# Kernel tuning notes

Measured on AMD Instinct MI355X. Metric: run time of the kernel, lower is better.

The kernel has to match this reference:

```python
import jax, jax.numpy as jnp
import numpy as np

NUM_CLASSES = 26
PERCENTILE = 95.0
BIG = jnp.float32(1e10)


def _erode(m):
    # scipy-style binary erosion with cross structuring element, border_value=0
    p = jnp.pad(m, 1, constant_values=False)
    return m & p[:-2, 1:-1] & p[2:, 1:-1] & p[1:-1, :-2] & p[1:-1, 2:]


def _boundary(m):
    return m & ~_erode(m)


def _edt(edge):
    # Exact Euclidean distance transform to nearest True pixel of `edge` [H, W].
    # Two-pass separable formulation (rows then columns), fully vectorized.
    H, W = edge.shape
    r = jnp.arange(H)
    rd2 = ((r[:, None] - r[None, :]) ** 2).astype(jnp.float32)  # [H, H']
    # g[i, j] = min over i' with edge[i', j] of (i - i')^2
    g = jnp.min(jnp.where(edge[None, :, :], rd2[:, :, None], BIG), axis=1)  # [H, W]
    c = jnp.arange(W)
    cd2 = ((c[:, None] - c[None, :]) ** 2).astype(jnp.float32)  # [W', W]
    # dt2[i, j] = min over j' of g[i, j'] + (j' - j)^2
    dt2 = jnp.min(g[:, :, None] + cd2[None, :, :], axis=1)  # [H, W]
    return jnp.sqrt(dt2)


def _pct95(dists, mask):
    # np.percentile(dists[mask], 95) with linear interpolation; nan if mask empty
    n = jnp.sum(mask)
    s = jnp.sort(jnp.where(mask, dists, jnp.inf))
    idx = (PERCENTILE / 100.0) * (n.astype(jnp.float32) - 1.0)
    idx = jnp.maximum(idx, 0.0)
    lo = jnp.floor(idx).astype(jnp.int32)
    hi = jnp.ceil(idx).astype(jnp.int32)
    vlo = s[lo]
    vhi = s[hi]
    val = vlo + (vhi - vlo) * (idx - jnp.floor(idx))
    return jnp.where(n > 0, val, jnp.nan)


def _hd_pair(pl, tl, c):
    # 95th-percentile symmetric Hausdorff between pred/target binary masks of class c
    pm = pl == c
    tm = tl == c
    pe = _boundary(pm)
    te = _boundary(tm)
    dt_t = _edt(te)  # distance to target boundary
    dt_p = _edt(pe)  # distance to pred boundary
    d_pt = _pct95(dt_t.ravel(), pe.ravel())  # pred-edge -> target-edge
    d_tp = _pct95(dt_p.ravel(), te.ravel())  # target-edge -> pred-edge
    return jnp.maximum(d_pt, d_tp)


def setup_inputs() -> dict:
    key = jax.random.key(0)
    k1, k2 = jax.random.split(key)
    predicted = jax.random.normal(k1, (2, NUM_CLASSES, 256, 256), dtype=jnp.float32)
    target = jax.random.normal(k2, (2, NUM_CLASSES, 256, 256), dtype=jnp.float32)
    return {"predicted": predicted, "target": target}


def reference(predicted, target):
    probs = jax.nn.softmax(predicted, axis=1)
    pl = jnp.argmax(probs, axis=1)   # [B, H, W]
    tl = jnp.argmax(target, axis=1)  # [B, H, W]

    def per_class(c):
        hd = jax.vmap(lambda p, t: _hd_pair(p, t, c))(pl, tl)  # [B]
        present = jnp.any(tl == c, axis=(1, 2))                # [B]
        return hd, present

    hds, pres = jax.lax.map(per_class, jnp.arange(NUM_CLASSES))  # [C, B]
    presf = pres.astype(jnp.float32)
    num = jnp.sum(jnp.where(pres, hds, 0.0), axis=0)  # [B]
    den = jnp.sum(presf, axis=0)                      # [B]
    batch_means = num / jnp.maximum(den, 1.0)
    valid = den > 0
    total = jnp.sum(jnp.where(valid, batch_means, 0.0)) / jnp.maximum(
        jnp.sum(valid.astype(jnp.float32)), 1.0)
    return jnp.where(jnp.any(valid), total, jnp.inf)
```

## Files before the change

kernel.cpp:

```cpp
#include <hip/hip_runtime.h>
#include <math.h>

#define HW 65536
#define NC 26
#define NB 2

#define PL_OFF    0
#define TL_OFF    131072
#define CNT_OFF   262144
#define RES_OFF   263424
#define BMP_OFF   264192
#define LISTP_OFF 1116160
#define LISTT_OFF 7931904
#define MINP_OFF  14747648
#define MINT_OFF  28379136

__global__ void k_labels(const float4* __restrict__ pred, const float4* __restrict__ targ,
                         uchar4* __restrict__ pl, uchar4* __restrict__ tl,
                         unsigned int* __restrict__ cnt) {
    int tid = threadIdx.x;
    if (blockIdx.x == 0) {
        for (int i = tid; i < 320; i += 128) cnt[i] = 0;
    }
    int idx = blockIdx.x * 128 + tid;
    if (idx >= (NB * HW / 4)) return;
    int b = idx >> 14, q = idx & 16383;
    const float4* p = pred + ((size_t)b * NC << 14) + q;
    const float4* t = targ + ((size_t)b * NC << 14) + q;
    float4 bp = p[0]; uchar4 ap = {0, 0, 0, 0};
    float4 bt = t[0]; uchar4 at = {0, 0, 0, 0};
#pragma unroll
    for (int c = 1; c < NC; ++c) {
        float4 vp = p[(size_t)c << 14];
        if (vp.x > bp.x) { bp.x = vp.x; ap.x = (unsigned char)c; }
        if (vp.y > bp.y) { bp.y = vp.y; ap.y = (unsigned char)c; }
        if (vp.z > bp.z) { bp.z = vp.z; ap.z = (unsigned char)c; }
        if (vp.w > bp.w) { bp.w = vp.w; ap.w = (unsigned char)c; }
        float4 vt = t[(size_t)c << 14];
        if (vt.x > bt.x) { bt.x = vt.x; at.x = (unsigned char)c; }
        if (vt.y > bt.y) { bt.y = vt.y; at.y = (unsigned char)c; }
        if (vt.z > bt.z) { bt.z = vt.z; at.z = (unsigned char)c; }
        if (vt.w > bt.w) { bt.w = vt.w; at.w = (unsigned char)c; }
    }
    pl[idx] = ap;
    tl[idx] = at;
}

__device__ __forceinline__ bool is_boundary(const unsigned char* __restrict__ L, int hw, int c) {
    int y = hw >> 8, x = hw & 255;
    if (y == 0 || y == 255 || x == 0 || x == 255) return true;
    return (int)L[hw - 256] != c || (int)L[hw + 256] != c ||
           (int)L[hw - 1]   != c || (int)L[hw + 1]   != c;
}

__global__ void k_rowbm(const unsigned char* __restrict__ pl,
                        const unsigned char* __restrict__ tl,
                        unsigned int* __restrict__ bmp,
                        unsigned int* __restrict__ cnt,
                        unsigned short* __restrict__ listP,
                        unsigned short* __restrict__ listT) {
    __shared__ unsigned bm[52][8];
    __shared__ unsigned lh[52];
    __shared__ unsigned lb[52];
    int tid = threadIdx.x;
    int b = blockIdx.x >> 8, y = blockIdx.x & 255;
    for (int i = tid; i < 416; i += 256) ((unsigned*)bm)[i] = 0;
    if (tid < 52) lh[tid] = 0;
    __syncthreads();
    const unsigned char* Lp = pl + (b << 16);
    const unsigned char* Lt = tl + (b << 16);
    int hw = (y << 8) | tid;
    int cp = Lp[hw];
    int ct = Lt[hw];
    bool bnp = is_boundary(Lp, hw, cp);
    bool bnt = is_boundary(Lt, hw, ct);
    unsigned rp = 0, rt = 0;
    if (bnp) {
        atomicOr(&bm[cp][tid >> 5], 1u << (tid & 31));
        rp = atomicAdd(&lh[cp], 1u);
    }
    if (bnt) {
        atomicOr(&bm[26 + ct][tid >> 5], 1u << (tid & 31));
        rt = atomicAdd(&lh[26 + ct], 1u);
    }
    __syncthreads();
    for (int i = tid; i < 416; i += 256) {
        int idx = i >> 3, w = i & 7;
        int m = idx < 26 ? 0 : 1;
        int c = idx < 26 ? idx : idx - 26;
        bmp[(((m * 52 + b * 26 + c) << 8) | y) * 8 + w] = bm[idx][w];
    }
    if (tid < 26)
        lb[tid] = lh[tid] ? atomicAdd(&cnt[208 + b * 26 + tid], lh[tid]) : 0u;
    else if (tid < 52)
        lb[tid] = lh[tid] ? atomicAdd(&cnt[260 + b * 26 + (tid - 26)], lh[tid]) : 0u;
    __syncthreads();
    if (bnp) listP[((unsigned)(b * 26 + cp) << 16) + lb[cp] + rp] = (unsigned short)hw;
    if (bnt) listT[((unsigned)(b * 26 + ct) << 16) + lb[26 + ct] + rt] = (unsigned short)hw;
}

__device__ __forceinline__ int row_dx(const unsigned* sb, int r, int xw, int xb) {
    const unsigned* row = sb + r * 9;
    unsigned RM = row[8];
    if (!RM) return 999;
    int dxmin = 999;
    unsigned m = row[xw];
    unsigned le = 0xFFFFFFFFu >> (31 - xb);
    unsigned lm = m & le;
    if (lm) dxmin = xb - 31 + __clz(lm);
    unsigned rmm = m & ~le;
    if (rmm) dxmin = min(dxmin, (__ffs(rmm) - 1) - xb);
    unsigned Lm = RM & ((1u << xw) - 1u);
    if (Lm) {
        int w1 = 31 - __clz(Lm);
        unsigned m1 = row[w1];
        dxmin = min(dxmin, xb + ((xw - w1) << 5) - (31 - __clz(m1)));
    }
    unsigned Rm = RM >> (xw + 1);
    if (Rm) {
        int w2 = xw + __ffs(Rm);
        unsigned m2 = row[w2];
        dxmin = min(dxmin, ((w2 - xw) << 5) + (__ffs(m2) - 1) - xb);
    }
    return dxmin;
}

__global__ __launch_bounds__(128) void k_ring(
        const unsigned int* __restrict__ cnt,
        const unsigned int* __restrict__ bmp,
        const unsigned short* __restrict__ listP,
        const unsigned short* __restrict__ listT,
        float* __restrict__ minP, float* __restrict__ minT) {
    int pair = blockIdx.y;
    int dir = blockIdx.z;
    unsigned ns = cnt[(dir ? 260 : 208) + pair];
    unsigned i0 = blockIdx.x * 128u;
    if (i0 >= ns) return;
    unsigned nt = cnt[(dir ? 208 : 260) + pair];
    if (nt == 0) return;
    const unsigned short* src = (dir ? listT : listP) + ((unsigned)pair << 16);
    float* outv = (dir ? minT : minP) + ((unsigned)pair << 16);

    __shared__ unsigned sb[256 * 9];
    int tid = threadIdx.x;
    {
        const uint4* g4 = (const uint4*)(bmp + ((unsigned)((dir ? 0 : 52) + pair) << 11));
#pragma unroll
        for (int t = 0; t < 4; ++t) {
            int idx = tid + t * 128;
            uint4 v = g4[idx];
            unsigned* row = sb + (idx >> 1) * 9 + ((idx & 1) << 2);
            row[0] = v.x; row[1] = v.y; row[2] = v.z; row[3] = v.w;
        }
    }
    __syncthreads();
    for (int r = tid; r < 256; r += 128) {
        const unsigned* row = sb + r * 9;
        unsigned rm = 0;
#pragma unroll
        for (int w = 0; w < 8; ++w) rm |= (row[w] ? 1u : 0u) << w;
        sb[r * 9 + 8] = rm;
    }
    __syncthreads();

    unsigned stride = gridDim.x * 128u;
    for (unsigned ib = i0; ib < ns; ib += stride) {
        unsigned i = ib + tid;
        if (i >= ns) continue;
        unsigned h = src[i];
        int x = (int)(h & 255u);
        int sy = (int)(h >> 8);
        int xw = x >> 5, xb = x & 31;
        int best = 0x40000000;
        for (int k = 0; k < 256; ++k) {
            int k2 = k * k;
            if (k2 >= best) break;
            int ra = sy - k, rb = sy + k;
            if (ra < 0 && rb > 255) break;
            if (ra >= 0) {
                int dx = row_dx(sb, ra, xw, xb);
                if (dx < 999) best = min(best, k2 + dx * dx);
            }
            if (k && rb < 256) {
                int dx = row_dx(sb, rb, xw, xb);
                if (dx < 999) best = min(best, k2 + dx * dx);
            }
        }
        outv[i] = (float)best;
    }
}

__global__ void k_select(const unsigned int* __restrict__ cnt,
                         const float* __restrict__ minP, const float* __restrict__ minT,
                         float* __restrict__ res) {
    int pair = blockIdx.x;
    int dir = blockIdx.y;
    unsigned ns = cnt[(dir ? 260 : 208) + pair];
    unsigned nt = cnt[(dir ? 208 : 260) + pair];
    const float* vals = (dir ? minT : minP) + ((unsigned)pair << 16);
    int tid = threadIdx.x;

    if (ns == 0) { if (tid == 0) res[pair * 2 + dir] = nanf(""); return; }
    if (nt == 0) { if (tid == 0) res[pair * 2 + dir] = sqrtf(1e10f); return; }

    __shared__ unsigned hist[1024];
    __shared__ unsigned f1[128], f2[128];
    __shared__ int s_binlo, s_binhi, s_below_lo, s_below_hi;

    for (int i = tid; i < 1024; i += 256) hist[i] = 0;
    __syncthreads();
    for (unsigned i = tid; i < ns; i += 256) {
        int v = (int)vals[i];
        atomicAdd(&hist[v >> 7], 1u);
    }
    __syncthreads();

    float idxf = 0.95f * ((float)ns - 1.0f);
    if (idxf < 0.f) idxf = 0.f;
    int klo = (int)floorf(idxf);
    int khi = (int)ceilf(idxf);

    if (tid == 0) {
        unsigned cum = 0;
        int binlo = -1, binhi = -1, below_lo = 0, below_hi = 0;
        for (int bkt = 0; bkt < 1024; ++bkt) {
            unsigned h = hist[bkt];
            if (binlo < 0 && cum + h > (unsigned)klo) { binlo = bkt; below_lo = (int)cum; }
            if (binhi < 0 && cum + h > (unsigned)khi) { binhi = bkt; below_hi = (int)cum; }
            cum += h;
            if (binhi >= 0) break;
        }
        s_binlo = binlo; s_binhi = binhi; s_below_lo = below_lo; s_below_hi = below_hi;
    }
    __syncthreads();
    if (tid < 128) { f1[tid] = 0; f2[tid] = 0; }
    __syncthreads();
    int binlo = s_binlo, binhi = s_binhi;
    for (unsigned i = tid; i < ns; i += 256) {
        int v = (int)vals[i];
        int bkt = v >> 7;
        if (bkt == binlo) atomicAdd(&f1[v & 127], 1u);
        if (bkt == binhi && binhi != binlo) atomicAdd(&f2[v & 127], 1u);
    }
    __syncthreads();
    if (tid == 0) {
        int rlo = klo - s_below_lo;
        unsigned cum = 0; int d2lo = binlo << 7, d2hi = binhi << 7;
        for (int j = 0; j < 128; ++j) {
            cum += f1[j];
            if ((int)cum > rlo) { d2lo = (binlo << 7) + j; break; }
        }
        if (binhi == binlo) {
            int rhi = khi - s_below_lo;
            cum = 0;
            for (int j = 0; j < 128; ++j) {
                cum += f1[j];
                if ((int)cum > rhi) { d2hi = (binlo << 7) + j; break; }
            }
        } else {
            int rhi = khi - s_below_hi;
            cum = 0;
            for (int j = 0; j < 128; ++j) {
                cum += f2[j];
                if ((int)cum > rhi) { d2hi = (binhi << 7) + j; break; }
            }
        }
        float vlo = sqrtf((float)d2lo);
        float vhi = sqrtf((float)d2hi);
        float frac = idxf - floorf(idxf);
        res[pair * 2 + dir] = vlo + (vhi - vlo) * frac;
    }
}

__global__ void k_final(const unsigned int* __restrict__ cnt, const float* __restrict__ res,
                        float* __restrict__ out) {
    __shared__ float s_res[104];
    __shared__ unsigned s_pres[52];
    int tid = threadIdx.x;
    if (tid < 104) s_res[tid] = res[tid];
    if (tid < 52) s_pres[tid] = cnt[260 + tid];
    __syncthreads();
    if (tid != 0) return;
    float total = 0.f, nvalid = 0.f;
    bool anyv = false;
    for (int b = 0; b < NB; ++b) {
        float num = 0.f, den = 0.f;
        for (int c = 0; c < NC; ++c) {
            int pair = b * NC + c;
            bool present = s_pres[pair] > 0;
            float dpt = s_res[pair * 2];
            float dtp = s_res[pair * 2 + 1];
            float hd;
            if (isnan(dpt) || isnan(dtp)) hd = nanf("");
            else hd = fmaxf(dpt, dtp);
            if (present) { num += hd; den += 1.f; }
        }
        float bm = num / fmaxf(den, 1.f);
        if (den > 0.f) { total += bm; nvalid += 1.f; anyv = true; }
    }
    out[0] = anyv ? (total / fmaxf(nvalid, 1.f)) : INFINITY;
}

extern "C" void kernel_launch(void* const* d_in, const int* in_sizes, int n_in,
                              void* d_out, int out_size, void* d_ws, size_t ws_size,
                              hipStream_t stream) {
    const float* pred = (const float*)d_in[0];
    const float* targ = (const float*)d_in[1];
    float* out = (float*)d_out;
    char* ws = (char*)d_ws;

    unsigned char* pl = (unsigned char*)(ws + PL_OFF);
    unsigned char* tl = (unsigned char*)(ws + TL_OFF);
    unsigned int* cnt = (unsigned int*)(ws + CNT_OFF);
    float* res = (float*)(ws + RES_OFF);
    unsigned int* bmp = (unsigned int*)(ws + BMP_OFF);
    unsigned short* listP = (unsigned short*)(ws + LISTP_OFF);
    unsigned short* listT = (unsigned short*)(ws + LISTT_OFF);
    float* minP = (float*)(ws + MINP_OFF);
    float* minT = (float*)(ws + MINT_OFF);

    k_labels<<<256, 128, 0, stream>>>((const float4*)pred, (const float4*)targ,
                                      (uchar4*)pl, (uchar4*)tl, cnt);
    k_rowbm<<<512, 256, 0, stream>>>(pl, tl, bmp, cnt, listP, listT);
    k_ring<<<dim3(24, 52, 2), 128, 0, stream>>>(cnt, bmp, listP, listT, minP, minT);
    k_select<<<dim3(52, 2), 256, 0, stream>>>(cnt, minP, minT, res);
    k_final<<<1, 128, 0, stream>>>(cnt, res, out);
}
```

Before: 47.02 us.

## Process two query points per thread in ring search and privatize select histogram

```diff
diff --git a/kernel.cpp b/kernel.cpp
--- a/kernel.cpp
+++ b/kernel.cpp
@@ -134,7 +134,7 @@
     int pair = blockIdx.y;
     int dir = blockIdx.z;
     unsigned ns = cnt[(dir ? 260 : 208) + pair];
-    unsigned i0 = blockIdx.x * 128u;
+    unsigned i0 = blockIdx.x * 256u;
     if (i0 >= ns) return;
     unsigned nt = cnt[(dir ? 208 : 260) + pair];
     if (nt == 0) return;
@@ -163,30 +163,47 @@
     }
     __syncthreads();
 
-    unsigned stride = gridDim.x * 128u;
+    unsigned stride = gridDim.x * 256u;
     for (unsigned ib = i0; ib < ns; ib += stride) {
-        unsigned i = ib + tid;
-        if (i >= ns) continue;
-        unsigned h = src[i];
-        int x = (int)(h & 255u);
-        int sy = (int)(h >> 8);
-        int xw = x >> 5, xb = x & 31;
-        int best = 0x40000000;
+        unsigned i_[2];
+        int sy[2], xw[2], xb[2], best[2];
+        bool valid[2];
+#pragma unroll
+        for (int j = 0; j < 2; ++j) {
+            unsigned i = ib + tid + (unsigned)(j << 7);
+            i_[j] = i;
+            valid[j] = i < ns;
+            if (valid[j]) {
+                unsigned h = src[i];
+                int x = (int)(h & 255u);
+                sy[j] = (int)(h >> 8);
+                xw[j] = x >> 5; xb[j] = x & 31;
+                best[j] = 0x40000000;
+            } else { sy[j] = 128; xw[j] = 0; xb[j] = 0; best[j] = 0; }
+        }
         for (int k = 0; k < 256; ++k) {
             int k2 = k * k;
-            if (k2 >= best) break;
-            int ra = sy - k, rb = sy + k;
-            if (ra < 0 && rb > 255) break;
-            if (ra >= 0) {
-                int dx = row_dx(sb, ra, xw, xb);
-                if (dx < 999) best = min(best, k2 + dx * dx);
+            bool done0 = (k2 >= best[0]) || (sy[0] - k < 0 && sy[0] + k > 255);
+            bool done1 = (k2 >= best[1]) || (sy[1] - k < 0 && sy[1] + k > 255);
+            if (done0 && done1) break;
+#pragma unroll
+            for (int j = 0; j < 2; ++j) {
+                if (k2 < best[j]) {
+                    int ra = sy[j] - k, rb = sy[j] + k;
+                    if (ra >= 0) {
+                        int dx = row_dx(sb, ra, xw[j], xb[j]);
+                        if (dx < 999) best[j] = min(best[j], k2 + dx * dx);
+                    }
+                    if (k && rb < 256) {
+                        int dx = row_dx(sb, rb, xw[j], xb[j]);
+                        if (dx < 999) best[j] = min(best[j], k2 + dx * dx);
+                    }
+                }
             }
-            if (k && rb < 256) {
-                int dx = row_dx(sb, rb, xw, xb);
-                if (dx < 999) best = min(best, k2 + dx * dx);
-            }
-        }
-        outv[i] = (float)best;
+        }
+#pragma unroll
+        for (int j = 0; j < 2; ++j)
+            if (valid[j]) outv[i_[j]] = (float)best[j];
     }
 }
 
@@ -203,15 +220,16 @@
     if (ns == 0) { if (tid == 0) res[pair * 2 + dir] = nanf(""); return; }
     if (nt == 0) { if (tid == 0) res[pair * 2 + dir] = sqrtf(1e10f); return; }
 
-    __shared__ unsigned hist[1024];
+    __shared__ unsigned hist4[4][1024];
     __shared__ unsigned f1[128], f2[128];
     __shared__ int s_binlo, s_binhi, s_below_lo, s_below_hi;
 
-    for (int i = tid; i < 1024; i += 256) hist[i] = 0;
-    __syncthreads();
+    for (int i = tid; i < 4096; i += 256) ((unsigned*)hist4)[i] = 0;
+    __syncthreads();
+    int sub = tid & 3;
     for (unsigned i = tid; i < ns; i += 256) {
         int v = (int)vals[i];
-        atomicAdd(&hist[v >> 7], 1u);
+        atomicAdd(&hist4[sub][v >> 7], 1u);
     }
     __syncthreads();
 
@@ -224,7 +242,7 @@
         unsigned cum = 0;
         int binlo = -1, binhi = -1, below_lo = 0, below_hi = 0;
         for (int bkt = 0; bkt < 1024; ++bkt) {
-            unsigned h = hist[bkt];
+            unsigned h = hist4[0][bkt] + hist4[1][bkt] + hist4[2][bkt] + hist4[3][bkt];
             if (binlo < 0 && cum + h > (unsigned)klo) { binlo = bkt; below_lo = (int)cum; }
             if (binhi < 0 && cum + h > (unsigned)khi) { binhi = bkt; below_hi = (int)cum; }
             cum += h;
@@ -322,7 +340,7 @@
     k_labels<<<256, 128, 0, stream>>>((const float4*)pred, (const float4*)targ,
                                       (uchar4*)pl, (uchar4*)tl, cnt);
     k_rowbm<<<512, 256, 0, stream>>>(pl, tl, bmp, cnt, listP, listT);
-    k_ring<<<dim3(24, 52, 2), 128, 0, stream>>>(cnt, bmp, listP, listT, minP, minT);
+    k_ring<<<dim3(12, 52, 2), 128, 0, stream>>>(cnt, bmp, listP, listT, minP, minT);
     k_select<<<dim3(52, 2), 256, 0, stream>>>(cnt, minP, minT, res);
     k_final<<<1, 128, 0, stream>>>(cnt, res, out);
 }
```

Measured after the change: 50.09 us. 6.5% more time.
